# Kernel tuning notes

Measured on AMD Instinct MI355X. Metric: run time of the kernel, lower is better.

The kernel has to match this reference:

```python
import jax, jax.numpy as jnp
import numpy as np

STUDENT_FRAMES = [0, 2, 4, 6]
EXTRA_FRAMES = [1, 3, 5, 7]       # teacher-only frames, sorted
SHARED_T = [2, 4, 6]              # shared frames in teacher indexing
SHARED_S = [1, 2, 3]              # same frames in student indexing
TOPK = 4
EPS = 1e-8                        # eps of _cos_angle's F.normalize
HUBER_DELTA = 1.0
A1 = A2 = A3 = 1.0


def _huber(pred, target, delta=HUBER_DELTA):
    err = pred - target
    ae = jnp.abs(err)
    return jnp.where(ae <= delta, 0.5 * err * err, delta * (ae - 0.5 * delta))


def _angles(h, r, c):
    """Cosine angles for the triangle (shared=h [B,F,S,D], ref=r [B,R,D], sim=c [B,R,K,D]).
    Expands cos(a-b, c-b) via pairwise dot products so no [.,.,.,.,D] tensor is materialized.
    Returns (a1, a2, a3) each of shape [B,F,R,S,K]."""
    ss = jnp.einsum('bfsd,brkd->bfrsk', h, c)   # shared . sim
    sr = jnp.einsum('bfsd,brd->bfrs', h, r)     # shared . ref
    rk = jnp.einsum('brd,brkd->brk', r, c)      # ref . sim
    rr = jnp.sum(r * r, -1)                     # [B,R]
    kk = jnp.sum(c * c, -1)                     # [B,R,K]
    hh = jnp.sum(h * h, -1)                     # [B,F,S]
    sr_ = sr[..., None]                         # bfrs1
    rk_ = rk[:, None, :, None, :]               # b1r1k
    rr_ = rr[:, None, :, None, None]            # b1r11
    kk_ = kk[:, None, :, None, :]               # b1r1k
    hh_ = hh[:, :, None, :, None]               # bf1s1
    n_hr = jnp.sqrt(jnp.maximum(hh_ + rr_ - 2.0 * sr_, 0.0))  # ||shared-ref||
    n_cr = jnp.sqrt(jnp.maximum(kk_ + rr_ - 2.0 * rk_, 0.0))  # ||sim-ref||
    n_hc = jnp.sqrt(jnp.maximum(hh_ + kk_ - 2.0 * ss, 0.0))   # ||shared-sim||
    def cos(num, na, nb):
        return num / (jnp.maximum(na, EPS) * jnp.maximum(nb, EPS))
    a1 = cos(ss - sr_ - rk_ + rr_, n_hr, n_cr)  # cos(shared-ref, sim-ref)
    a2 = cos(sr_ - rk_ - ss + kk_, n_cr, n_hc)  # cos(ref-sim, shared-sim)
    a3 = cos(rk_ - sr_ - ss + hh_, n_hr, n_hc)  # cos(ref-shared, sim-shared)
    return a1, a2, a3


def setup_inputs() -> dict:
    key = jax.random.key(0)
    k1, k2, k3, k4 = jax.random.split(key, 4)
    B, V, P, D = 4, 8, 1369, 2048
    teacher_feats = jax.random.normal(k1, (B, V, P, D), jnp.float32)
    student_feats = jax.random.normal(k2, (B, len(STUDENT_FRAMES), P, D), jnp.float32)
    ref_perm = jax.random.permutation(k3, P)[:128].astype(jnp.int32)
    shared_perm = jax.random.permutation(k4, P)[:128].astype(jnp.int32)
    return {'teacher_feats': teacher_feats, 'student_feats': student_feats,
            'ref_perm': ref_perm, 'shared_perm': shared_perm}


def reference(teacher_feats, student_feats, ref_perm, shared_perm):
    teacher = jax.lax.stop_gradient(teacher_feats)  # teacher side is fully detached
    B, V, P, D = teacher.shape

    ref_t = teacher[:, STUDENT_FRAMES[0], ref_perm, :]        # [B,R,D]
    ref_s = student_feats[:, 0, ref_perm, :]                  # [B,R,D]

    # extra (teacher-only) frames concatenated along patches -> [B, 4*P, D]
    extra_t = teacher[:, jnp.array(EXTRA_FRAMES)].reshape(B, len(EXTRA_FRAMES) * P, D)

    # cosine similarity + topk selection (selection_mode='topk')
    ref_tn = ref_t / jnp.maximum(jnp.linalg.norm(ref_t, axis=-1, keepdims=True), 1e-12)
    extra_tn = extra_t / jnp.maximum(jnp.linalg.norm(extra_t, axis=-1, keepdims=True), 1e-12)
    sim = jnp.einsum('brd,bed->bre', ref_tn, extra_tn)        # [B,R,4P]
    _, idx = jax.lax.top_k(sim, TOPK)                         # [B,R,K]
    sim_high = jax.vmap(lambda e, i: e[i])(extra_t, idx)      # [B,R,K,D]

    shared_t = teacher[:, jnp.array(SHARED_T)][:, :, shared_perm, :]        # [B,F,S,D]
    shared_s = student_feats[:, jnp.array(SHARED_S)][:, :, shared_perm, :]  # [B,F,S,D]

    a1_t, a2_t, a3_t = _angles(shared_t, ref_t, sim_high)
    a1_s, a2_s, a3_s = _angles(shared_s, ref_s, sim_high)

    l1 = _huber(a1_s, a1_t).mean()
    l2 = _huber(a2_s, a2_t).mean()
    l3 = _huber(a3_s, a3_t).mean()
    loss = A1 * l1 + A2 * l2 + A3 * l3
    return loss
```

## Files before the change

### kernel.cpp

```cpp
#include <hip/hip_runtime.h>

#define B_ 4
#define V_ 8
#define P_ 1369
#define D_ 2048
#define R_ 128
#define F_ 3
#define K_ 4
#define E_ 5476
#define CAND_ 8
#define EPS_ 1e-8f

typedef unsigned short u16;
typedef __attribute__((ext_vector_type(8))) short bf16x8;
typedef __attribute__((ext_vector_type(4))) float f32x4;

__device__ inline u16 f2bf(float f){
  unsigned int u = __float_as_uint(f);
  u = u + 0x7fffu + ((u >> 16) & 1u);
  return (u16)(u >> 16);
}
__device__ inline int pack2bf(float lo, float hi){
  return (int)(((unsigned)f2bf(hi) << 16) | (unsigned)f2bf(lo));
}
__device__ inline float sq8(float4 a, float4 b){
  return a.x*a.x + a.y*a.y + a.z*a.z + a.w*a.w
       + b.x*b.x + b.y*b.y + b.z*b.z + b.w*b.w;
}
__device__ inline float huber1(float e){
  float ae = fabsf(e);
  return ae <= 1.0f ? 0.5f*e*e : (ae - 0.5f);
}
__device__ inline float blk_sum(float v, float* scr){
  for (int off = 32; off; off >>= 1) v += __shfl_xor(v, off, 64);
  __syncthreads();
  if ((threadIdx.x & 63) == 0) scr[threadIdx.x >> 6] = v;
  __syncthreads();
  float s = scr[0] + scr[1] + scr[2] + scr[3];
  __syncthreads();
  return s;
}

__global__ __launch_bounds__(256) void k_prep(
    const float* __restrict__ teacher, const float* __restrict__ student,
    const int* __restrict__ ref_perm, const int* __restrict__ shared_perm,
    u16* __restrict__ ref_tn, float* __restrict__ rr_t, float* __restrict__ rr_s,
    u16* __restrict__ shT, u16* __restrict__ shS,
    float* __restrict__ hhT, float* __restrict__ hhS){
  __shared__ float scr[4];
  int t = threadIdx.x;
  if (blockIdx.x < 512){
    int br = blockIdx.x, b = br >> 7, r = br & 127;
    int p = ref_perm[r];
    const float* tp = teacher + ((size_t)(b*V_)*P_ + p)*D_;
    const float* sp = student + ((size_t)(b*4)*P_ + p)*D_;
    float4 x0 = *(const float4*)(tp + t*8);
    float4 x1 = *(const float4*)(tp + t*8 + 4);
    float sumt = blk_sum(sq8(x0, x1), scr);
    float4 y0 = *(const float4*)(sp + t*8);
    float4 y1 = *(const float4*)(sp + t*8 + 4);
    float sums = blk_sum(sq8(y0, y1), scr);
    if (t == 0){ rr_t[br] = sumt; rr_s[br] = sums; }
    float inv = 1.0f / fmaxf(sqrtf(sumt), 1e-12f);
    int4 pt = { pack2bf(x0.x*inv, x0.y*inv), pack2bf(x0.z*inv, x0.w*inv),
                pack2bf(x1.x*inv, x1.y*inv), pack2bf(x1.z*inv, x1.w*inv) };
    *(int4*)(ref_tn + (size_t)br*D_ + t*8) = pt;
  } else {
    int id = blockIdx.x - 512;
    int b = id / 384, fs = id % 384;
    int f = fs >> 7, s = fs & 127;
    int p = shared_perm[s];
    const float* tp = teacher + ((size_t)(b*V_ + 2 + 2*f)*P_ + p)*D_;
    const float* sp = student + ((size_t)(b*4 + 1 + f)*P_ + p)*D_;
    float4 x0 = *(const float4*)(tp + t*8);
    float4 x1 = *(const float4*)(tp + t*8 + 4);
    float sumt = blk_sum(sq8(x0, x1), scr);
    int4 pt = { pack2bf(x0.x, x0.y), pack2bf(x0.z, x0.w),
                pack2bf(x1.x, x1.y), pack2bf(x1.z, x1.w) };
    *(int4*)(shT + (size_t)id*D_ + t*8) = pt;
    float4 y0 = *(const float4*)(sp + t*8);
    float4 y1 = *(const float4*)(sp + t*8 + 4);
    float sums = blk_sum(sq8(y0, y1), scr);
    int4 ps = { pack2bf(y0.x, y0.y), pack2bf(y0.z, y0.w),
                pack2bf(y1.x, y1.y), pack2bf(y1.z, y1.w) };
    *(int4*)(shS + (size_t)id*D_ + t*8) = ps;
    if (t == 0){ hhT[id] = sumt; hhS[id] = sums; }
  }
}

__global__ __launch_bounds__(256) void k_sim(
    const float* __restrict__ teacher, const u16* __restrict__ ref_tn,
    float* __restrict__ sim){
  __shared__ __align__(16) u16 As[128][72];
  __shared__ __align__(16) u16 Bs[64][72];
  __shared__ float nsq[64];
  int b = blockIdx.y;
  int e0 = blockIdx.x * 64;
  int t = threadIdx.x, lane = t & 63, w = t >> 6, wm = w >> 1, wn = w & 1;
  f32x4 acc[4][2];
  for (int i = 0; i < 4; i++)
    for (int j = 0; j < 2; j++)
      acc[i][j] = (f32x4){0.f, 0.f, 0.f, 0.f};
  int arow = t >> 1, acol = (t & 1) * 32;
  int brow = t >> 2, bcol = (t & 3) * 16;
  int e = e0 + brow;
  const u16* asrc = ref_tn + ((size_t)(b*128 + arow))*D_ + acol;
  const float* bsrc = nullptr;
  if (e < E_) bsrc = teacher + ((size_t)(b*V_ + 1 + 2*(e / P_))*P_ + (e % P_))*D_ + bcol;
  float q = 0.0f;
  int lr = lane & 15;
  for (int k0 = 0; k0 < D_; k0 += 64){
    __syncthreads();
#pragma unroll
    for (int u = 0; u < 4; u++)
      *(int4*)&As[arow][acol + u*8] = *(const int4*)(asrc + k0 + u*8);
    float4 z0, z1, z2, z3;
    if (bsrc){
      z0 = *(const float4*)(bsrc + k0);      z1 = *(const float4*)(bsrc + k0 + 4);
      z2 = *(const float4*)(bsrc + k0 + 8);  z3 = *(const float4*)(bsrc + k0 + 12);
    } else {
      z0 = make_float4(0.f,0.f,0.f,0.f); z1 = z0; z2 = z0; z3 = z0;
    }
    q += sq8(z0, z1) + sq8(z2, z3);
    int4 p0 = { pack2bf(z0.x, z0.y), pack2bf(z0.z, z0.w),
                pack2bf(z1.x, z1.y), pack2bf(z1.z, z1.w) };
    int4 p1 = { pack2bf(z2.x, z2.y), pack2bf(z2.z, z2.w),
                pack2bf(z3.x, z3.y), pack2bf(z3.z, z3.w) };
    *(int4*)&Bs[brow][bcol]     = p0;
    *(int4*)&Bs[brow][bcol + 8] = p1;
    __syncthreads();
#pragma unroll
    for (int kk = 0; kk < 2; kk++){
      int kof = kk*32 + (lane >> 4) * 8;
      bf16x8 bf0 = *(const bf16x8*)&Bs[wn*32 + lr][kof];
      bf16x8 bf1 = *(const bf16x8*)&Bs[wn*32 + 16 + lr][kof];
#pragma unroll
      for (int mi = 0; mi < 4; mi++){
        bf16x8 af = *(const bf16x8*)&As[wm*64 + mi*16 + lr][kof];
        acc[mi][0] = __builtin_amdgcn_mfma_f32_16x16x32_bf16(af, bf0, acc[mi][0], 0, 0, 0);
        acc[mi][1] = __builtin_amdgcn_mfma_f32_16x16x32_bf16(af, bf1, acc[mi][1], 0, 0, 0);
      }
    }
  }
  q += __shfl_xor(q, 1, 64);
  q += __shfl_xor(q, 2, 64);
  if ((t & 3) == 0) nsq[t >> 2] = q;
  __syncthreads();
  int lg = lane >> 4;
#pragma unroll
  for (int mi = 0; mi < 4; mi++){
#pragma unroll
    for (int ni = 0; ni < 2; ni++){
      int el = wn*32 + ni*16 + lr;
      int e_idx = e0 + el;
      if (e_idx < E_){
        float inv = 1.0f / fmaxf(sqrtf(nsq[el]), 1e-12f);
#pragma unroll
        for (int reg = 0; reg < 4; reg++){
          int r_idx = wm*64 + mi*16 + lg*4 + reg;
          sim[((size_t)(b*128 + r_idx))*E_ + e_idx] = acc[mi][ni][reg] * inv;
        }
      }
    }
  }
}

__global__ __launch_bounds__(256) void k_rescore(
    const float* __restrict__ teacher, const float* __restrict__ student,
    const int* __restrict__ ref_perm, const float* __restrict__ sim,
    const float* __restrict__ rr_t,
    u16* __restrict__ packT, u16* __restrict__ packS,
    float* __restrict__ kkw, float* __restrict__ rkT, float* __restrict__ rkS){
  __shared__ float v[E_];
  __shared__ float rT[D_];
  __shared__ float rS[D_];
  __shared__ float rv[4];
  __shared__ int ri[4];
  __shared__ int cand[CAND_];
  __shared__ float csim[CAND_], cq[CAND_], cdT[CAND_];
  __shared__ int order[4];
  int br = blockIdx.x, b = br >> 7, r = br & 127, t = threadIdx.x;
  int lane = t & 63, w = t >> 6;
  const float* row = sim + (size_t)br*E_;
  for (int i = t; i < E_; i += 256) v[i] = row[i];
  __syncthreads();
  for (int c = 0; c < CAND_; c++){
    float bv = -3.4e38f;
    int bi = 0x7fffffff;
    for (int i = t; i < E_; i += 256){
      float x = v[i];
      if (x > bv){ bv = x; bi = i; }
    }
    for (int off = 32; off; off >>= 1){
      float ov = __shfl_down(bv, off, 64);
      int   oi = __shfl_down(bi, off, 64);
      if (ov > bv || (ov == bv && oi < bi)){ bv = ov; bi = oi; }
    }
    if (lane == 0){ rv[w] = bv; ri[w] = bi; }
    __syncthreads();
    if (t == 0){
      for (int w2 = 1; w2 < 4; w2++)
        if (rv[w2] > rv[0] || (rv[w2] == rv[0] && ri[w2] < ri[0])){ rv[0] = rv[w2]; ri[0] = ri[w2]; }
      cand[c] = ri[0];
      v[ri[0]] = -3.4e38f;
    }
    __syncthreads();
  }
  int p = ref_perm[r];
  const float* tp = teacher + ((size_t)(b*V_)*P_ + p)*D_;
  const float* sp = student + ((size_t)(b*4)*P_ + p)*D_;
  float4 x0 = *(const float4*)(tp + t*8);
  float4 x1 = *(const float4*)(tp + t*8 + 4);
  float4 y0 = *(const float4*)(sp + t*8);
  float4 y1 = *(const float4*)(sp + t*8 + 4);
  *(float4*)&rT[t*8]   = x0; *(float4*)&rT[t*8+4] = x1;
  *(float4*)&rS[t*8]   = y0; *(float4*)&rS[t*8+4] = y1;
  {
    int4 pt = { pack2bf(x0.x, x0.y), pack2bf(x0.z, x0.w),
                pack2bf(x1.x, x1.y), pack2bf(x1.z, x1.w) };
    *(int4*)(packT + ((size_t)(br*5 + 4))*D_ + t*8) = pt;
    int4 ps = { pack2bf(y0.x, y0.y), pack2bf(y0.z, y0.w),
                pack2bf(y1.x, y1.y), pack2bf(y1.z, y1.w) };
    *(int4*)(packS + ((size_t)(br*5 + 4))*D_ + t*8) = ps;
  }
  float invt = 1.0f / fmaxf(sqrtf(rr_t[br]), 1e-12f);
  __syncthreads();
  for (int c = w; c < CAND_; c += 4){
    int e = cand[c];
    const float* xp = teacher + ((size_t)(b*V_ + 1 + 2*(e / P_))*P_ + (e % P_))*D_;
    float d = 0.f, q = 0.f;
#pragma unroll
    for (int j = 0; j < 32; j++){
      float xv = xp[lane + 64*j];
      d += xv * rT[lane + 64*j];
      q += xv * xv;
    }
    for (int off = 32; off; off >>= 1){
      d += __shfl_xor(d, off, 64);
      q += __shfl_xor(q, off, 64);
    }
    if (lane == 0){
      cdT[c] = d; cq[c] = q;
      csim[c] = d * invt / fmaxf(sqrtf(q), 1e-12f);
    }
  }
  __syncthreads();
  if (t == 0){
    unsigned used = 0;
    for (int k = 0; k < 4; k++){
      int best = -1;
      for (int c = 0; c < CAND_; c++){
        if (used & (1u << c)) continue;
        if (best < 0){ best = c; continue; }
        if (csim[c] > csim[best] ||
            (csim[c] == csim[best] && cand[c] < cand[best])) best = c;
      }
      used |= 1u << best;
      order[k] = best;
    }
  }
  __syncthreads();
  {
    int c = order[w];
    int e = cand[c];
    const float* xp = teacher + ((size_t)(b*V_ + 1 + 2*(e / P_))*P_ + (e % P_))*D_;
    float ds = 0.f;
#pragma unroll
    for (int j = 0; j < 32; j++)
      ds += xp[lane + 64*j] * rS[lane + 64*j];
    for (int off = 32; off; off >>= 1) ds += __shfl_xor(ds, off, 64);
    if (lane == 0){
      kkw[br*4 + w] = cq[c];
      rkT[br*4 + w] = cdT[c];
      rkS[br*4 + w] = ds;
    }
    const float* src = xp + lane*32;
#pragma unroll
    for (int u = 0; u < 4; u++){
      float4 a  = *(const float4*)(src + u*8);
      float4 b2 = *(const float4*)(src + u*8 + 4);
      int4 pc = { pack2bf(a.x, a.y), pack2bf(a.z, a.w),
                  pack2bf(b2.x, b2.y), pack2bf(b2.z, b2.w) };
      size_t po = ((size_t)(br*5 + w))*D_ + lane*32 + u*8;
      *(int4*)(packT + po) = pc;
      *(int4*)(packS + po) = pc;
    }
  }
}

__global__ __launch_bounds__(256) void k_angle_gemm(
    const u16* __restrict__ shT, const u16* __restrict__ shS,
    const u16* __restrict__ packT, const u16* __restrict__ packS,
    float* __restrict__ outT, float* __restrict__ outS){
  __shared__ __align__(16) u16 As[128][72];
  __shared__ __align__(16) u16 Bs[64][72];
  int which = blockIdx.z;
  const u16* A  = which ? shS : shT;
  const u16* Bp = which ? packS : packT;
  float* out = which ? outS : outT;
  int b = blockIdx.y;
  int mt = blockIdx.x % 3, nt = blockIdx.x / 3;
  int m0 = mt*128, n0 = nt*64;
  int t = threadIdx.x, lane = t & 63, w = t >> 6, wm = w >> 1, wn = w & 1;
  f32x4 acc[4][2];
  for (int i = 0; i < 4; i++)
    for (int j = 0; j < 2; j++)
      acc[i][j] = (f32x4){0.f, 0.f, 0.f, 0.f};
  int arow = t >> 1, acol = (t & 1) * 32;
  int brow = t >> 2, bcol = (t & 3) * 16;
  const u16* asrc = A  + ((size_t)(b*384 + m0 + arow))*D_ + acol;
  const u16* bsrc = Bp + ((size_t)(b*640 + n0 + brow))*D_ + bcol;
  int lr = lane & 15;
  for (int k0 = 0; k0 < D_; k0 += 64){
    __syncthreads();
#pragma unroll
    for (int u = 0; u < 4; u++)
      *(int4*)&As[arow][acol + u*8] = *(const int4*)(asrc + k0 + u*8);
    *(int4*)&Bs[brow][bcol]     = *(const int4*)(bsrc + k0);
    *(int4*)&Bs[brow][bcol + 8] = *(const int4*)(bsrc + k0 + 8);
    __syncthreads();
#pragma unroll
    for (int kk = 0; kk < 2; kk++){
      int kof = kk*32 + (lane >> 4) * 8;
      bf16x8 bf0 = *(const bf16x8*)&Bs[wn*32 + lr][kof];
      bf16x8 bf1 = *(const bf16x8*)&Bs[wn*32 + 16 + lr][kof];
#pragma unroll
      for (int mi = 0; mi < 4; mi++){
        bf16x8 af = *(const bf16x8*)&As[wm*64 + mi*16 + lr][kof];
        acc[mi][0] = __builtin_amdgcn_mfma_f32_16x16x32_bf16(af, bf0, acc[mi][0], 0, 0, 0);
        acc[mi][1] = __builtin_amdgcn_mfma_f32_16x16x32_bf16(af, bf1, acc[mi][1], 0, 0, 0);
      }
    }
  }
  int lg = lane >> 4;
#pragma unroll
  for (int mi = 0; mi < 4; mi++)
#pragma unroll
    for (int ni = 0; ni < 2; ni++)
#pragma unroll
      for (int reg = 0; reg < 4; reg++){
        int r_idx = wm*64 + mi*16 + lg*4 + reg;
        int c_idx = wn*32 + ni*16 + lr;
        out[((size_t)(b*384 + m0 + r_idx))*640 + n0 + c_idx] = acc[mi][ni][reg];
      }
}

__global__ __launch_bounds__(256) void k_assemble(
    const float* __restrict__ outT, const float* __restrict__ outS,
    const float* __restrict__ hhT, const float* __restrict__ hhS,
    const float* __restrict__ rrT, const float* __restrict__ rrS,
    const float* __restrict__ kkw, const float* __restrict__ rkT, const float* __restrict__ rkS,
    double* __restrict__ partials){
  __shared__ double dscr[4];
  int idx = blockIdx.x*256 + threadIdx.x;
  int r = idx & 127, s = (idx >> 7) & 127, bf = idx >> 14;
  int f = bf % 3, b = bf / 3;
  int fs = f*128 + s;
  const float* oT = outT + ((size_t)(b*384 + fs))*640 + r*5;
  const float* oS = outS + ((size_t)(b*384 + fs))*640 + r*5;
  float hh_t = hhT[b*384 + fs], hh_s = hhS[b*384 + fs];
  float rr_tv = rrT[b*128 + r], rr_sv = rrS[b*128 + r];
  float sr_t = oT[4], sr_s = oS[4];
  float nhr_t = sqrtf(fmaxf(hh_t + rr_tv - 2.0f*sr_t, 0.0f));
  float nhr_s = sqrtf(fmaxf(hh_s + rr_sv - 2.0f*sr_s, 0.0f));
  float h1 = 0.f, h2 = 0.f, h3 = 0.f;
#pragma unroll
  for (int k = 0; k < 4; k++){
    float ss_t = oT[k], ss_s = oS[k];
    float kk = kkw[(b*128 + r)*4 + k];
    float rk_t = rkT[(b*128 + r)*4 + k];
    float rk_s = rkS[(b*128 + r)*4 + k];
    float ncr_t = sqrtf(fmaxf(kk + rr_tv - 2.0f*rk_t, 0.0f));
    float ncr_s = sqrtf(fmaxf(kk + rr_sv - 2.0f*rk_s, 0.0f));
    float nhc_t = sqrtf(fmaxf(hh_t + kk - 2.0f*ss_t, 0.0f));
    float nhc_s = sqrtf(fmaxf(hh_s + kk - 2.0f*ss_s, 0.0f));
    float a1t = (ss_t - sr_t - rk_t + rr_tv) / (fmaxf(nhr_t, EPS_) * fmaxf(ncr_t, EPS_));
    float a2t = (sr_t - rk_t - ss_t + kk)    / (fmaxf(ncr_t, EPS_) * fmaxf(nhc_t, EPS_));
    float a3t = (rk_t - sr_t - ss_t + hh_t)  / (fmaxf(nhr_t, EPS_) * fmaxf(nhc_t, EPS_));
    float a1s = (ss_s - sr_s - rk_s + rr_sv) / (fmaxf(nhr_s, EPS_) * fmaxf(ncr_s, EPS_));
    float a2s = (sr_s - rk_s - ss_s + kk)    / (fmaxf(ncr_s, EPS_) * fmaxf(nhc_s, EPS_));
    float a3s = (rk_s - sr_s - ss_s + hh_s)  / (fmaxf(nhr_s, EPS_) * fmaxf(nhc_s, EPS_));
    h1 += huber1(a1s - a1t);
    h2 += huber1(a2s - a2t);
    h3 += huber1(a3s - a3t);
  }
  double d1 = h1, d2 = h2, d3 = h3;
  for (int off = 32; off; off >>= 1){
    d1 += __shfl_xor(d1, off, 64);
    d2 += __shfl_xor(d2, off, 64);
    d3 += __shfl_xor(d3, off, 64);
  }
  int w = threadIdx.x >> 6;
  if ((threadIdx.x & 63) == 0) dscr[w] = d1;
  __syncthreads();
  if (threadIdx.x == 0) partials[blockIdx.x*3 + 0] = dscr[0]+dscr[1]+dscr[2]+dscr[3];
  __syncthreads();
  if ((threadIdx.x & 63) == 0) dscr[w] = d2;
  __syncthreads();
  if (threadIdx.x == 0) partials[blockIdx.x*3 + 1] = dscr[0]+dscr[1]+dscr[2]+dscr[3];
  __syncthreads();
  if ((threadIdx.x & 63) == 0) dscr[w] = d3;
  __syncthreads();
  if (threadIdx.x == 0) partials[blockIdx.x*3 + 2] = dscr[0]+dscr[1]+dscr[2]+dscr[3];
}

__global__ __launch_bounds__(256) void k_final(
    const double* __restrict__ partials, float* __restrict__ out){
  __shared__ double dscr[12];
  int t = threadIdx.x;
  double l1 = 0, l2 = 0, l3 = 0;
  for (int i = t; i < 768; i += 256){
    l1 += partials[i*3 + 0];
    l2 += partials[i*3 + 1];
    l3 += partials[i*3 + 2];
  }
  for (int off = 32; off; off >>= 1){
    l1 += __shfl_xor(l1, off, 64);
    l2 += __shfl_xor(l2, off, 64);
    l3 += __shfl_xor(l3, off, 64);
  }
  int w = t >> 6;
  if ((t & 63) == 0){ dscr[w*3] = l1; dscr[w*3+1] = l2; dscr[w*3+2] = l3; }
  __syncthreads();
  if (t == 0){
    double L1 = dscr[0] + dscr[3] + dscr[6] + dscr[9];
    double L2 = dscr[1] + dscr[4] + dscr[7] + dscr[10];
    double L3 = dscr[2] + dscr[5] + dscr[8] + dscr[11];
    out[0] = (float)((L1 + L2 + L3) / 786432.0);
  }
}

extern "C" void kernel_launch(void* const* d_in, const int* in_sizes, int n_in,
                              void* d_out, int out_size, void* d_ws, size_t ws_size,
                              hipStream_t stream){
  (void)in_sizes; (void)n_in; (void)out_size; (void)ws_size;
  const float* teacher = (const float*)d_in[0];
  const float* student = (const float*)d_in[1];
  const int* ref_perm = (const int*)d_in[2];
  const int* shared_perm = (const int*)d_in[3];
  float* out = (float*)d_out;

  char* ws = (char*)d_ws;
  size_t off = 0;
  auto alloc = [&](size_t bytes)->char*{
    char* pp = ws + off;
    off += (bytes + 255) & ~(size_t)255;
    return pp;
  };
  u16*    ref_tn  = (u16*)   alloc((size_t)B_*R_*D_*sizeof(u16));
  float*  rr_t    = (float*) alloc(B_*R_*sizeof(float));
  float*  rr_s    = (float*) alloc(B_*R_*sizeof(float));
  float*  kkw     = (float*) alloc(B_*R_*K_*sizeof(float));
  float*  rkT     = (float*) alloc(B_*R_*K_*sizeof(float));
  float*  rkS     = (float*) alloc(B_*R_*K_*sizeof(float));
  u16*    shT     = (u16*)   alloc((size_t)B_*384*D_*sizeof(u16));
  u16*    shS     = (u16*)   alloc((size_t)B_*384*D_*sizeof(u16));
  float*  hhT     = (float*) alloc(B_*384*sizeof(float));
  float*  hhS     = (float*) alloc(B_*384*sizeof(float));
  float*  outT    = (float*) alloc((size_t)B_*384*640*sizeof(float));
  float*  outS    = (float*) alloc((size_t)B_*384*640*sizeof(float));
  double* partials= (double*)alloc(768*3*sizeof(double));
  float*  sim     = (float*) alloc((size_t)B_*R_*E_*sizeof(float));
  u16*    packT   = (u16*)   alloc((size_t)B_*R_*5*D_*sizeof(u16));
  u16*    packS   = (u16*)   alloc((size_t)B_*R_*5*D_*sizeof(u16));

  k_prep<<<dim3(2048), dim3(256), 0, stream>>>(teacher, student, ref_perm, shared_perm,
                                               ref_tn, rr_t, rr_s, shT, shS, hhT, hhS);
  k_sim<<<dim3((E_ + 63)/64, B_), dim3(256), 0, stream>>>(teacher, ref_tn, sim);
  k_rescore<<<dim3(B_*R_), dim3(256), 0, stream>>>(teacher, student, ref_perm, sim, rr_t,
                                                   packT, packS, kkw, rkT, rkS);
  k_angle_gemm<<<dim3(30, B_, 2), dim3(256), 0, stream>>>(shT, shS, packT, packS, outT, outS);
  k_assemble<<<dim3(768), dim3(256), 0, stream>>>(outT, outS, hhT, hhS, rr_t, rr_s, kkw, rkT, rkS, partials);
  k_final<<<dim3(1), dim3(256), 0, stream>>>(partials, out);
}
```

Baseline: 149.4 us.

## Shrink GEMM tiles for more blocks and cache per-thread maxima in top-k selection

The sim GEMM moves to 32-column tiles, which doubles its grid, and the angle GEMM moves to 64x64 tiles, also doubling its grid, so more of the many CUs get work. The candidate selection in k_rescore now scans the row once to keep a per-thread running maximum. After each pick, only the thread that owned the winner rescans its strided slice, instead of all threads rescanning the whole row eight times. Smaller tiles reduce operand reuse per block, so A-tile loads per useful MFMA go up and may add memory traffic.

```diff
diff --git a/kernel.cpp b/kernel.cpp
--- a/kernel.cpp
+++ b/kernel.cpp
@@ -92,17 +92,17 @@
     const float* __restrict__ teacher, const u16* __restrict__ ref_tn,
     float* __restrict__ sim){
   __shared__ __align__(16) u16 As[128][72];
-  __shared__ __align__(16) u16 Bs[64][72];
-  __shared__ float nsq[64];
+  __shared__ __align__(16) u16 Bs[32][72];
+  __shared__ float nsq[32];
   int b = blockIdx.y;
-  int e0 = blockIdx.x * 64;
-  int t = threadIdx.x, lane = t & 63, w = t >> 6, wm = w >> 1, wn = w & 1;
-  f32x4 acc[4][2];
-  for (int i = 0; i < 4; i++)
+  int e0 = blockIdx.x * 32;
+  int t = threadIdx.x, lane = t & 63, w = t >> 6;
+  f32x4 acc[2][2];
+  for (int i = 0; i < 2; i++)
     for (int j = 0; j < 2; j++)
       acc[i][j] = (f32x4){0.f, 0.f, 0.f, 0.f};
   int arow = t >> 1, acol = (t & 1) * 32;
-  int brow = t >> 2, bcol = (t & 3) * 16;
+  int brow = t >> 3, bcol = (t & 7) * 8;
   int e = e0 + brow;
   const u16* asrc = ref_tn + ((size_t)(b*128 + arow))*D_ + acol;
   const float* bsrc = nullptr;
@@ -114,29 +114,22 @@
 #pragma unroll
     for (int u = 0; u < 4; u++)
       *(int4*)&As[arow][acol + u*8] = *(const int4*)(asrc + k0 + u*8);
-    float4 z0, z1, z2, z3;
-    if (bsrc){
-      z0 = *(const float4*)(bsrc + k0);      z1 = *(const float4*)(bsrc + k0 + 4);
-      z2 = *(const float4*)(bsrc + k0 + 8);  z3 = *(const float4*)(bsrc + k0 + 12);
-    } else {
-      z0 = make_float4(0.f,0.f,0.f,0.f); z1 = z0; z2 = z0; z3 = z0;
-    }
-    q += sq8(z0, z1) + sq8(z2, z3);
+    float4 z0, z1;
+    if (bsrc){ z0 = *(const float4*)(bsrc + k0); z1 = *(const float4*)(bsrc + k0 + 4); }
+    else { z0 = make_float4(0.f,0.f,0.f,0.f); z1 = z0; }
+    q += sq8(z0, z1);
     int4 p0 = { pack2bf(z0.x, z0.y), pack2bf(z0.z, z0.w),
                 pack2bf(z1.x, z1.y), pack2bf(z1.z, z1.w) };
-    int4 p1 = { pack2bf(z2.x, z2.y), pack2bf(z2.z, z2.w),
-                pack2bf(z3.x, z3.y), pack2bf(z3.z, z3.w) };
-    *(int4*)&Bs[brow][bcol]     = p0;
-    *(int4*)&Bs[brow][bcol + 8] = p1;
+    *(int4*)&Bs[brow][bcol] = p0;
     __syncthreads();
 #pragma unroll
     for (int kk = 0; kk < 2; kk++){
       int kof = kk*32 + (lane >> 4) * 8;
-      bf16x8 bf0 = *(const bf16x8*)&Bs[wn*32 + lr][kof];
-      bf16x8 bf1 = *(const bf16x8*)&Bs[wn*32 + 16 + lr][kof];
-#pragma unroll
-      for (int mi = 0; mi < 4; mi++){
-        bf16x8 af = *(const bf16x8*)&As[wm*64 + mi*16 + lr][kof];
+      bf16x8 bf0 = *(const bf16x8*)&Bs[lr][kof];
+      bf16x8 bf1 = *(const bf16x8*)&Bs[16 + lr][kof];
+#pragma unroll
+      for (int mi = 0; mi < 2; mi++){
+        bf16x8 af = *(const bf16x8*)&As[w*32 + mi*16 + lr][kof];
         acc[mi][0] = __builtin_amdgcn_mfma_f32_16x16x32_bf16(af, bf0, acc[mi][0], 0, 0, 0);
         acc[mi][1] = __builtin_amdgcn_mfma_f32_16x16x32_bf16(af, bf1, acc[mi][1], 0, 0, 0);
       }
@@ -144,20 +137,21 @@
   }
   q += __shfl_xor(q, 1, 64);
   q += __shfl_xor(q, 2, 64);
-  if ((t & 3) == 0) nsq[t >> 2] = q;
+  q += __shfl_xor(q, 4, 64);
+  if ((t & 7) == 0) nsq[t >> 3] = q;
   __syncthreads();
   int lg = lane >> 4;
 #pragma unroll
-  for (int mi = 0; mi < 4; mi++){
+  for (int mi = 0; mi < 2; mi++){
 #pragma unroll
     for (int ni = 0; ni < 2; ni++){
-      int el = wn*32 + ni*16 + lr;
+      int el = ni*16 + lr;
       int e_idx = e0 + el;
       if (e_idx < E_){
         float inv = 1.0f / fmaxf(sqrtf(nsq[el]), 1e-12f);
 #pragma unroll
         for (int reg = 0; reg < 4; reg++){
-          int r_idx = wm*64 + mi*16 + lg*4 + reg;
+          int r_idx = w*32 + mi*16 + lg*4 + reg;
           sim[((size_t)(b*128 + r_idx))*E_ + e_idx] = acc[mi][ni][reg] * inv;
         }
       }
@@ -174,6 +168,8 @@
   __shared__ float v[E_];
   __shared__ float rT[D_];
   __shared__ float rS[D_];
+  __shared__ float tv[256];
+  __shared__ int   ti[256];
   __shared__ float rv[4];
   __shared__ int ri[4];
   __shared__ int cand[CAND_];
@@ -184,25 +180,39 @@
   const float* row = sim + (size_t)br*E_;
   for (int i = t; i < E_; i += 256) v[i] = row[i];
   __syncthreads();
-  for (int c = 0; c < CAND_; c++){
-    float bv = -3.4e38f;
-    int bi = 0x7fffffff;
+  {
+    float bv = -3.4e38f; int bi = 0x7fffffff;
     for (int i = t; i < E_; i += 256){
       float x = v[i];
       if (x > bv){ bv = x; bi = i; }
     }
+    tv[t] = bv; ti[t] = bi;
+  }
+  __syncthreads();
+  for (int c = 0; c < CAND_; c++){
+    float mv = tv[t]; int mi2 = ti[t];
     for (int off = 32; off; off >>= 1){
-      float ov = __shfl_down(bv, off, 64);
-      int   oi = __shfl_down(bi, off, 64);
-      if (ov > bv || (ov == bv && oi < bi)){ bv = ov; bi = oi; }
-    }
-    if (lane == 0){ rv[w] = bv; ri[w] = bi; }
+      float ov = __shfl_down(mv, off, 64);
+      int   oi = __shfl_down(mi2, off, 64);
+      if (ov > mv || (ov == mv && oi < mi2)){ mv = ov; mi2 = oi; }
+    }
+    if (lane == 0){ rv[w] = mv; ri[w] = mi2; }
     __syncthreads();
     if (t == 0){
       for (int w2 = 1; w2 < 4; w2++)
         if (rv[w2] > rv[0] || (rv[w2] == rv[0] && ri[w2] < ri[0])){ rv[0] = rv[w2]; ri[0] = ri[w2]; }
       cand[c] = ri[0];
       v[ri[0]] = -3.4e38f;
+    }
+    __syncthreads();
+    int win = cand[c];
+    if (t == (win & 255)){
+      float nb = -3.4e38f; int nbi = 0x7fffffff;
+      for (int i = t; i < E_; i += 256){
+        float x = v[i];
+        if (x > nb){ nb = x; nbi = i; }
+      }
+      tv[t] = nb; ti[t] = nbi;
     }
     __syncthreads();
   }
@@ -292,32 +302,30 @@
     const u16* __restrict__ shT, const u16* __restrict__ shS,
     const u16* __restrict__ packT, const u16* __restrict__ packS,
     float* __restrict__ outT, float* __restrict__ outS){
-  __shared__ __align__(16) u16 As[128][72];
+  __shared__ __align__(16) u16 As[64][72];
   __shared__ __align__(16) u16 Bs[64][72];
   int which = blockIdx.z;
   const u16* A  = which ? shS : shT;
   const u16* Bp = which ? packS : packT;
   float* out = which ? outS : outT;
   int b = blockIdx.y;
-  int mt = blockIdx.x % 3, nt = blockIdx.x / 3;
-  int m0 = mt*128, n0 = nt*64;
+  int mt = blockIdx.x % 6, nt = blockIdx.x / 6;
+  int m0 = mt*64, n0 = nt*64;
   int t = threadIdx.x, lane = t & 63, w = t >> 6, wm = w >> 1, wn = w & 1;
-  f32x4 acc[4][2];
-  for (int i = 0; i < 4; i++)
+  f32x4 acc[2][2];
+  for (int i = 0; i < 2; i++)
     for (int j = 0; j < 2; j++)
       acc[i][j] = (f32x4){0.f, 0.f, 0.f, 0.f};
-  int arow = t >> 1, acol = (t & 1) * 32;
-  int brow = t >> 2, bcol = (t & 3) * 16;
+  int arow = t >> 2, acol = (t & 3) * 16;
   const u16* asrc = A  + ((size_t)(b*384 + m0 + arow))*D_ + acol;
-  const u16* bsrc = Bp + ((size_t)(b*640 + n0 + brow))*D_ + bcol;
+  const u16* bsrc = Bp + ((size_t)(b*640 + n0 + arow))*D_ + acol;
   int lr = lane & 15;
   for (int k0 = 0; k0 < D_; k0 += 64){
     __syncthreads();
-#pragma unroll
-    for (int u = 0; u < 4; u++)
-      *(int4*)&As[arow][acol + u*8] = *(const int4*)(asrc + k0 + u*8);
-    *(int4*)&Bs[brow][bcol]     = *(const int4*)(bsrc + k0);
-    *(int4*)&Bs[brow][bcol + 8] = *(const int4*)(bsrc + k0 + 8);
+    *(int4*)&As[arow][acol]     = *(const int4*)(asrc + k0);
+    *(int4*)&As[arow][acol + 8] = *(const int4*)(asrc + k0 + 8);
+    *(int4*)&Bs[arow][acol]     = *(const int4*)(bsrc + k0);
+    *(int4*)&Bs[arow][acol + 8] = *(const int4*)(bsrc + k0 + 8);
     __syncthreads();
 #pragma unroll
     for (int kk = 0; kk < 2; kk++){
@@ -325,8 +333,8 @@
       bf16x8 bf0 = *(const bf16x8*)&Bs[wn*32 + lr][kof];
       bf16x8 bf1 = *(const bf16x8*)&Bs[wn*32 + 16 + lr][kof];
 #pragma unroll
-      for (int mi = 0; mi < 4; mi++){
-        bf16x8 af = *(const bf16x8*)&As[wm*64 + mi*16 + lr][kof];
+      for (int mi = 0; mi < 2; mi++){
+        bf16x8 af = *(const bf16x8*)&As[wm*32 + mi*16 + lr][kof];
         acc[mi][0] = __builtin_amdgcn_mfma_f32_16x16x32_bf16(af, bf0, acc[mi][0], 0, 0, 0);
         acc[mi][1] = __builtin_amdgcn_mfma_f32_16x16x32_bf16(af, bf1, acc[mi][1], 0, 0, 0);
       }
@@ -334,12 +342,12 @@
   }
   int lg = lane >> 4;
 #pragma unroll
-  for (int mi = 0; mi < 4; mi++)
+  for (int mi = 0; mi < 2; mi++)
 #pragma unroll
     for (int ni = 0; ni < 2; ni++)
 #pragma unroll
       for (int reg = 0; reg < 4; reg++){
-        int r_idx = wm*64 + mi*16 + lg*4 + reg;
+        int r_idx = wm*32 + mi*16 + lg*4 + reg;
         int c_idx = wn*32 + ni*16 + lr;
         out[((size_t)(b*384 + m0 + r_idx))*640 + n0 + c_idx] = acc[mi][ni][reg];
       }
@@ -466,10 +474,10 @@
 
   k_prep<<<dim3(2048), dim3(256), 0, stream>>>(teacher, student, ref_perm, shared_perm,
                                                ref_tn, rr_t, rr_s, shT, shS, hhT, hhS);
-  k_sim<<<dim3((E_ + 63)/64, B_), dim3(256), 0, stream>>>(teacher, ref_tn, sim);
+  k_sim<<<dim3((E_ + 31)/32, B_), dim3(256), 0, stream>>>(teacher, ref_tn, sim);
   k_rescore<<<dim3(B_*R_), dim3(256), 0, stream>>>(teacher, student, ref_perm, sim, rr_t,
                                                    packT, packS, kkw, rkT, rkS);
-  k_angle_gemm<<<dim3(30, B_, 2), dim3(256), 0, stream>>>(shT, shS, packT, packS, outT, outS);
+  k_angle_gemm<<<dim3(60, B_, 2), dim3(256), 0, stream>>>(shT, shS, packT, packS, outT, outS);
   k_assemble<<<dim3(768), dim3(256), 0, stream>>>(outT, outS, hhT, hhS, rr_t, rr_s, kkw, rkT, rkS, partials);
   k_final<<<dim3(1), dim3(256), 0, stream>>>(partials, out);
 }
```

After: 160.2 us. 7.2% more time.

## Split-K the similarity GEMM, fuse shared-frame prep into it, speed candidate selection

Applied to the files above, without the earlier changes.

The similarity GEMM is split into two K halves, doubling the block count to fill more CUs. Each half writes unnormalized partial sums and partial squared norms, which the rescore kernel adds and normalizes. The shared-frame conversion blocks now run in the same launch as the GEMM, so they overlap with it. Candidate selection keeps per-thread maxima in shared memory and rescans only the winning thread's stripe each round instead of a full block scan. The cost is twice the sim buffer writes and reads, plus an extra launch for the ref prep.

```diff
diff --git a/kernel.cpp b/kernel.cpp
--- a/kernel.cpp
+++ b/kernel.cpp
@@ -10,6 +10,8 @@
 #define E_ 5476
 #define CAND_ 8
 #define EPS_ 1e-8f
+#define ETILES_ 86
+#define SIMBLK_ (ETILES_*B_*2)
 
 typedef unsigned short u16;
 typedef __attribute__((ext_vector_type(8))) short bf16x8;
@@ -41,32 +43,111 @@
   return s;
 }
 
-__global__ __launch_bounds__(256) void k_prep(
+__global__ __launch_bounds__(256) void k_prep_ref(
     const float* __restrict__ teacher, const float* __restrict__ student,
-    const int* __restrict__ ref_perm, const int* __restrict__ shared_perm,
-    u16* __restrict__ ref_tn, float* __restrict__ rr_t, float* __restrict__ rr_s,
+    const int* __restrict__ ref_perm,
+    u16* __restrict__ ref_tn, float* __restrict__ rr_t, float* __restrict__ rr_s){
+  __shared__ float scr[4];
+  int br = blockIdx.x, b = br >> 7, r = br & 127, t = threadIdx.x;
+  int p = ref_perm[r];
+  const float* tp = teacher + ((size_t)(b*V_)*P_ + p)*D_;
+  const float* sp = student + ((size_t)(b*4)*P_ + p)*D_;
+  float4 x0 = *(const float4*)(tp + t*8);
+  float4 x1 = *(const float4*)(tp + t*8 + 4);
+  float sumt = blk_sum(sq8(x0, x1), scr);
+  float4 y0 = *(const float4*)(sp + t*8);
+  float4 y1 = *(const float4*)(sp + t*8 + 4);
+  float sums = blk_sum(sq8(y0, y1), scr);
+  if (t == 0){ rr_t[br] = sumt; rr_s[br] = sums; }
+  float inv = 1.0f / fmaxf(sqrtf(sumt), 1e-12f);
+  int4 pt = { pack2bf(x0.x*inv, x0.y*inv), pack2bf(x0.z*inv, x0.w*inv),
+              pack2bf(x1.x*inv, x1.y*inv), pack2bf(x1.z*inv, x1.w*inv) };
+  *(int4*)(ref_tn + (size_t)br*D_ + t*8) = pt;
+}
+
+__global__ __launch_bounds__(256) void k_sim_fused(
+    const float* __restrict__ teacher, const float* __restrict__ student,
+    const u16* __restrict__ ref_tn, const int* __restrict__ shared_perm,
+    float* __restrict__ simPart, float* __restrict__ nsqPart,
     u16* __restrict__ shT, u16* __restrict__ shS,
     float* __restrict__ hhT, float* __restrict__ hhS){
-  __shared__ float scr[4];
-  int t = threadIdx.x;
-  if (blockIdx.x < 512){
-    int br = blockIdx.x, b = br >> 7, r = br & 127;
-    int p = ref_perm[r];
-    const float* tp = teacher + ((size_t)(b*V_)*P_ + p)*D_;
-    const float* sp = student + ((size_t)(b*4)*P_ + p)*D_;
-    float4 x0 = *(const float4*)(tp + t*8);
-    float4 x1 = *(const float4*)(tp + t*8 + 4);
-    float sumt = blk_sum(sq8(x0, x1), scr);
-    float4 y0 = *(const float4*)(sp + t*8);
-    float4 y1 = *(const float4*)(sp + t*8 + 4);
-    float sums = blk_sum(sq8(y0, y1), scr);
-    if (t == 0){ rr_t[br] = sumt; rr_s[br] = sums; }
-    float inv = 1.0f / fmaxf(sqrtf(sumt), 1e-12f);
-    int4 pt = { pack2bf(x0.x*inv, x0.y*inv), pack2bf(x0.z*inv, x0.w*inv),
-                pack2bf(x1.x*inv, x1.y*inv), pack2bf(x1.z*inv, x1.w*inv) };
-    *(int4*)(ref_tn + (size_t)br*D_ + t*8) = pt;
+  __shared__ __align__(16) u16 As[128][72];
+  __shared__ __align__(16) u16 Bs[64][72];
+  __shared__ float scr4[4];
+  int bx = blockIdx.x, t = threadIdx.x;
+  if (bx < SIMBLK_){
+    int h = bx / (ETILES_*B_);
+    int rem = bx % (ETILES_*B_);
+    int b = rem / ETILES_, et = rem % ETILES_;
+    int e0 = et * 64;
+    int lane = t & 63, w = t >> 6, wm = w >> 1, wn = w & 1;
+    f32x4 acc[4][2];
+    for (int i = 0; i < 4; i++)
+      for (int j = 0; j < 2; j++)
+        acc[i][j] = (f32x4){0.f, 0.f, 0.f, 0.f};
+    int arow = t >> 1, acol = (t & 1) * 32;
+    int brow = t >> 2, bcol = (t & 3) * 16;
+    int e = e0 + brow;
+    const u16* asrc = ref_tn + ((size_t)(b*128 + arow))*D_ + acol;
+    const float* bsrc = nullptr;
+    if (e < E_) bsrc = teacher + ((size_t)(b*V_ + 1 + 2*(e / P_))*P_ + (e % P_))*D_ + bcol;
+    float q = 0.0f;
+    int lr = lane & 15;
+    int kbeg = h * 1024, kend = kbeg + 1024;
+    for (int k0 = kbeg; k0 < kend; k0 += 64){
+      __syncthreads();
+#pragma unroll
+      for (int u = 0; u < 4; u++)
+        *(int4*)&As[arow][acol + u*8] = *(const int4*)(asrc + k0 + u*8);
+      float4 z0, z1, z2, z3;
+      if (bsrc){
+        z0 = *(const float4*)(bsrc + k0);      z1 = *(const float4*)(bsrc + k0 + 4);
+        z2 = *(const float4*)(bsrc + k0 + 8);  z3 = *(const float4*)(bsrc + k0 + 12);
+      } else {
+        z0 = make_float4(0.f,0.f,0.f,0.f); z1 = z0; z2 = z0; z3 = z0;
+      }
+      q += sq8(z0, z1) + sq8(z2, z3);
+      int4 p0 = { pack2bf(z0.x, z0.y), pack2bf(z0.z, z0.w),
+                  pack2bf(z1.x, z1.y), pack2bf(z1.z, z1.w) };
+      int4 p1 = { pack2bf(z2.x, z2.y), pack2bf(z2.z, z2.w),
+                  pack2bf(z3.x, z3.y), pack2bf(z3.z, z3.w) };
+      *(int4*)&Bs[brow][bcol]     = p0;
+      *(int4*)&Bs[brow][bcol + 8] = p1;
+      __syncthreads();
+#pragma unroll
+      for (int kk = 0; kk < 2; kk++){
+        int kof = kk*32 + (lane >> 4) * 8;
+        bf16x8 bf0 = *(const bf16x8*)&Bs[wn*32 + lr][kof];
+        bf16x8 bf1 = *(const bf16x8*)&Bs[wn*32 + 16 + lr][kof];
+#pragma unroll
+        for (int mi = 0; mi < 4; mi++){
+          bf16x8 af = *(const bf16x8*)&As[wm*64 + mi*16 + lr][kof];
+          acc[mi][0] = __builtin_amdgcn_mfma_f32_16x16x32_bf16(af, bf0, acc[mi][0], 0, 0, 0);
+          acc[mi][1] = __builtin_amdgcn_mfma_f32_16x16x32_bf16(af, bf1, acc[mi][1], 0, 0, 0);
+        }
+      }
+    }
+    q += __shfl_xor(q, 1, 64);
+    q += __shfl_xor(q, 2, 64);
+    if ((t & 3) == 0 && e < E_) nsqPart[(size_t)(h*4 + b)*E_ + e] = q;
+    int lg = lane >> 4;
+#pragma unroll
+    for (int mi = 0; mi < 4; mi++){
+#pragma unroll
+      for (int ni = 0; ni < 2; ni++){
+        int el = wn*32 + ni*16 + lr;
+        int e_idx = e0 + el;
+        if (e_idx < E_){
+#pragma unroll
+          for (int reg = 0; reg < 4; reg++){
+            int r_idx = wm*64 + mi*16 + lg*4 + reg;
+            simPart[((size_t)((h*4 + b)*128 + r_idx))*E_ + e_idx] = acc[mi][ni][reg];
+          }
+        }
+      }
+    }
   } else {
-    int id = blockIdx.x - 512;
+    int id = bx - SIMBLK_;
     int b = id / 384, fs = id % 384;
     int f = fs >> 7, s = fs & 127;
     int p = shared_perm[s];
@@ -74,13 +155,13 @@
     const float* sp = student + ((size_t)(b*4 + 1 + f)*P_ + p)*D_;
     float4 x0 = *(const float4*)(tp + t*8);
     float4 x1 = *(const float4*)(tp + t*8 + 4);
-    float sumt = blk_sum(sq8(x0, x1), scr);
+    float sumt = blk_sum(sq8(x0, x1), scr4);
     int4 pt = { pack2bf(x0.x, x0.y), pack2bf(x0.z, x0.w),
                 pack2bf(x1.x, x1.y), pack2bf(x1.z, x1.w) };
     *(int4*)(shT + (size_t)id*D_ + t*8) = pt;
     float4 y0 = *(const float4*)(sp + t*8);
     float4 y1 = *(const float4*)(sp + t*8 + 4);
-    float sums = blk_sum(sq8(y0, y1), scr);
+    float sums = blk_sum(sq8(y0, y1), scr4);
     int4 ps = { pack2bf(y0.x, y0.y), pack2bf(y0.z, y0.w),
                 pack2bf(y1.x, y1.y), pack2bf(y1.z, y1.w) };
     *(int4*)(shS + (size_t)id*D_ + t*8) = ps;
@@ -88,92 +169,18 @@
   }
 }
 
-__global__ __launch_bounds__(256) void k_sim(
-    const float* __restrict__ teacher, const u16* __restrict__ ref_tn,
-    float* __restrict__ sim){
-  __shared__ __align__(16) u16 As[128][72];
-  __shared__ __align__(16) u16 Bs[64][72];
-  __shared__ float nsq[64];
-  int b = blockIdx.y;
-  int e0 = blockIdx.x * 64;
-  int t = threadIdx.x, lane = t & 63, w = t >> 6, wm = w >> 1, wn = w & 1;
-  f32x4 acc[4][2];
-  for (int i = 0; i < 4; i++)
-    for (int j = 0; j < 2; j++)
-      acc[i][j] = (f32x4){0.f, 0.f, 0.f, 0.f};
-  int arow = t >> 1, acol = (t & 1) * 32;
-  int brow = t >> 2, bcol = (t & 3) * 16;
-  int e = e0 + brow;
-  const u16* asrc = ref_tn + ((size_t)(b*128 + arow))*D_ + acol;
-  const float* bsrc = nullptr;
-  if (e < E_) bsrc = teacher + ((size_t)(b*V_ + 1 + 2*(e / P_))*P_ + (e % P_))*D_ + bcol;
-  float q = 0.0f;
-  int lr = lane & 15;
-  for (int k0 = 0; k0 < D_; k0 += 64){
-    __syncthreads();
-#pragma unroll
-    for (int u = 0; u < 4; u++)
-      *(int4*)&As[arow][acol + u*8] = *(const int4*)(asrc + k0 + u*8);
-    float4 z0, z1, z2, z3;
-    if (bsrc){
-      z0 = *(const float4*)(bsrc + k0);      z1 = *(const float4*)(bsrc + k0 + 4);
-      z2 = *(const float4*)(bsrc + k0 + 8);  z3 = *(const float4*)(bsrc + k0 + 12);
-    } else {
-      z0 = make_float4(0.f,0.f,0.f,0.f); z1 = z0; z2 = z0; z3 = z0;
-    }
-    q += sq8(z0, z1) + sq8(z2, z3);
-    int4 p0 = { pack2bf(z0.x, z0.y), pack2bf(z0.z, z0.w),
-                pack2bf(z1.x, z1.y), pack2bf(z1.z, z1.w) };
-    int4 p1 = { pack2bf(z2.x, z2.y), pack2bf(z2.z, z2.w),
-                pack2bf(z3.x, z3.y), pack2bf(z3.z, z3.w) };
-    *(int4*)&Bs[brow][bcol]     = p0;
-    *(int4*)&Bs[brow][bcol + 8] = p1;
-    __syncthreads();
-#pragma unroll
-    for (int kk = 0; kk < 2; kk++){
-      int kof = kk*32 + (lane >> 4) * 8;
-      bf16x8 bf0 = *(const bf16x8*)&Bs[wn*32 + lr][kof];
-      bf16x8 bf1 = *(const bf16x8*)&Bs[wn*32 + 16 + lr][kof];
-#pragma unroll
-      for (int mi = 0; mi < 4; mi++){
-        bf16x8 af = *(const bf16x8*)&As[wm*64 + mi*16 + lr][kof];
-        acc[mi][0] = __builtin_amdgcn_mfma_f32_16x16x32_bf16(af, bf0, acc[mi][0], 0, 0, 0);
-        acc[mi][1] = __builtin_amdgcn_mfma_f32_16x16x32_bf16(af, bf1, acc[mi][1], 0, 0, 0);
-      }
-    }
-  }
-  q += __shfl_xor(q, 1, 64);
-  q += __shfl_xor(q, 2, 64);
-  if ((t & 3) == 0) nsq[t >> 2] = q;
-  __syncthreads();
-  int lg = lane >> 4;
-#pragma unroll
-  for (int mi = 0; mi < 4; mi++){
-#pragma unroll
-    for (int ni = 0; ni < 2; ni++){
-      int el = wn*32 + ni*16 + lr;
-      int e_idx = e0 + el;
-      if (e_idx < E_){
-        float inv = 1.0f / fmaxf(sqrtf(nsq[el]), 1e-12f);
-#pragma unroll
-        for (int reg = 0; reg < 4; reg++){
-          int r_idx = wm*64 + mi*16 + lg*4 + reg;
-          sim[((size_t)(b*128 + r_idx))*E_ + e_idx] = acc[mi][ni][reg] * inv;
-        }
-      }
-    }
-  }
-}
-
 __global__ __launch_bounds__(256) void k_rescore(
     const float* __restrict__ teacher, const float* __restrict__ student,
-    const int* __restrict__ ref_perm, const float* __restrict__ sim,
+    const int* __restrict__ ref_perm,
+    const float* __restrict__ simPart, const float* __restrict__ nsqPart,
     const float* __restrict__ rr_t,
     u16* __restrict__ packT, u16* __restrict__ packS,
     float* __restrict__ kkw, float* __restrict__ rkT, float* __restrict__ rkS){
   __shared__ float v[E_];
   __shared__ float rT[D_];
   __shared__ float rS[D_];
+  __shared__ float tv[256];
+  __shared__ int   ti[256];
   __shared__ float rv[4];
   __shared__ int ri[4];
   __shared__ int cand[CAND_];
@@ -181,28 +188,49 @@
   __shared__ int order[4];
   int br = blockIdx.x, b = br >> 7, r = br & 127, t = threadIdx.x;
   int lane = t & 63, w = t >> 6;
-  const float* row = sim + (size_t)br*E_;
-  for (int i = t; i < E_; i += 256) v[i] = row[i];
-  __syncthreads();
-  for (int c = 0; c < CAND_; c++){
-    float bv = -3.4e38f;
-    int bi = 0x7fffffff;
+  const float* p0 = simPart + ((size_t)(b*128 + r))*E_;
+  const float* p1 = simPart + ((size_t)((4 + b)*128 + r))*E_;
+  const float* q0 = nsqPart + (size_t)b*E_;
+  const float* q1 = nsqPart + (size_t)(4 + b)*E_;
+  for (int i = t; i < E_; i += 256){
+    float qq = q0[i] + q1[i];
+    float inv = 1.0f / fmaxf(sqrtf(qq), 1e-12f);
+    v[i] = (p0[i] + p1[i]) * inv;
+  }
+  __syncthreads();
+  {
+    float bv = -3.4e38f; int bi = 0x7fffffff;
     for (int i = t; i < E_; i += 256){
       float x = v[i];
       if (x > bv){ bv = x; bi = i; }
     }
+    tv[t] = bv; ti[t] = bi;
+  }
+  __syncthreads();
+  for (int c = 0; c < CAND_; c++){
+    float mv = tv[t]; int mi2 = ti[t];
     for (int off = 32; off; off >>= 1){
-      float ov = __shfl_down(bv, off, 64);
-      int   oi = __shfl_down(bi, off, 64);
-      if (ov > bv || (ov == bv && oi < bi)){ bv = ov; bi = oi; }
-    }
-    if (lane == 0){ rv[w] = bv; ri[w] = bi; }
+      float ov = __shfl_down(mv, off, 64);
+      int   oi = __shfl_down(mi2, off, 64);
+      if (ov > mv || (ov == mv && oi < mi2)){ mv = ov; mi2 = oi; }
+    }
+    if (lane == 0){ rv[w] = mv; ri[w] = mi2; }
     __syncthreads();
     if (t == 0){
       for (int w2 = 1; w2 < 4; w2++)
         if (rv[w2] > rv[0] || (rv[w2] == rv[0] && ri[w2] < ri[0])){ rv[0] = rv[w2]; ri[0] = ri[w2]; }
       cand[c] = ri[0];
       v[ri[0]] = -3.4e38f;
+    }
+    __syncthreads();
+    int win = cand[c];
+    if (t == (win & 255)){
+      float nb = -3.4e38f; int nbi = 0x7fffffff;
+      for (int i = t; i < E_; i += 256){
+        float x = v[i];
+        if (x > nb){ nb = x; nbi = i; }
+      }
+      tv[t] = nb; ti[t] = nbi;
     }
     __syncthreads();
   }
@@ -460,14 +488,17 @@
   float*  outT    = (float*) alloc((size_t)B_*384*640*sizeof(float));
   float*  outS    = (float*) alloc((size_t)B_*384*640*sizeof(float));
   double* partials= (double*)alloc(768*3*sizeof(double));
-  float*  sim     = (float*) alloc((size_t)B_*R_*E_*sizeof(float));
+  float*  simPart = (float*) alloc((size_t)2*B_*R_*E_*sizeof(float));
+  float*  nsqPart = (float*) alloc((size_t)2*B_*E_*sizeof(float));
   u16*    packT   = (u16*)   alloc((size_t)B_*R_*5*D_*sizeof(u16));
   u16*    packS   = (u16*)   alloc((size_t)B_*R_*5*D_*sizeof(u16));
 
-  k_prep<<<dim3(2048), dim3(256), 0, stream>>>(teacher, student, ref_perm, shared_perm,
-                                               ref_tn, rr_t, rr_s, shT, shS, hhT, hhS);
-  k_sim<<<dim3((E_ + 63)/64, B_), dim3(256), 0, stream>>>(teacher, ref_tn, sim);
-  k_rescore<<<dim3(B_*R_), dim3(256), 0, stream>>>(teacher, student, ref_perm, sim, rr_t,
+  k_prep_ref<<<dim3(B_*R_), dim3(256), 0, stream>>>(teacher, student, ref_perm,
+                                                    ref_tn, rr_t, rr_s);
+  k_sim_fused<<<dim3(SIMBLK_ + 1536), dim3(256), 0, stream>>>(
+      teacher, student, ref_tn, shared_perm, simPart, nsqPart, shT, shS, hhT, hhS);
+  k_rescore<<<dim3(B_*R_), dim3(256), 0, stream>>>(teacher, student, ref_perm,
+                                                   simPart, nsqPart, rr_t,
                                                    packT, packS, kkw, rkT, rkS);
   k_angle_gemm<<<dim3(30, B_, 2), dim3(256), 0, stream>>>(shT, shS, packT, packS, outT, outS);
   k_assemble<<<dim3(768), dim3(256), 0, stream>>>(outT, outS, hhT, hhS, rr_t, rr_s, kkw, rkT, rkS, partials);
```

Result: faster. 133.8 us (-10.5%).
